# Kernel tuning notes

Hardware: AMD Instinct MI355X
Metric: run time of the kernel (lower is better)

The kernel has to match this reference:

```python
import jax, jax.numpy as jnp
import numpy as np

D_MODEL = 1024
H = 16
DK = D_MODEL // H
S = 4096


def setup_inputs() -> dict:
    key = jax.random.key(0)
    ks = jax.random.split(key, 11)
    scale = 1.0 / np.sqrt(D_MODEL)
    return {
        "Q": jax.random.normal(ks[0], (S, D_MODEL), jnp.float32),
        "K": jax.random.normal(ks[1], (S, D_MODEL), jnp.float32),
        "V": jax.random.normal(ks[2], (S, D_MODEL), jnp.float32),
        # per-head projection weights, stacked: [h, d_model, d_k]
        "Wq": jax.random.normal(ks[3], (H, D_MODEL, DK), jnp.float32) * scale,
        "bq": jax.random.normal(ks[4], (H, DK), jnp.float32) * 0.01,
        "Wk": jax.random.normal(ks[5], (H, D_MODEL, DK), jnp.float32) * scale,
        "bk": jax.random.normal(ks[6], (H, DK), jnp.float32) * 0.01,
        "Wv": jax.random.normal(ks[7], (H, D_MODEL, DK), jnp.float32) * scale,
        "bv": jax.random.normal(ks[8], (H, DK), jnp.float32) * 0.01,
        # output projection (torch Linear convention: y = x @ Wo.T + bo)
        "Wo": jax.random.normal(ks[9], (D_MODEL, D_MODEL), jnp.float32) * scale,
        "bo": jax.random.normal(ks[10], (D_MODEL,), jnp.float32) * 0.01,
    }


def reference(Q, K, V, Wq, bq, Wk, bk, Wv, bv, Wo, bo):
    # per-head projections, vectorized over heads: [h, S, d_k]
    q = jnp.einsum("sd,hdk->hsk", Q, Wq) + bq[:, None, :]
    k = jnp.einsum("sd,hdk->hsk", K, Wk) + bk[:, None, :]
    v = jnp.einsum("sd,hdk->hsk", V, Wv) + bv[:, None, :]
    # scaled dot-product attention (full [h, S, S] scores, as in the original)
    scores = jnp.einsum("hsk,htk->hst", q, k) / jnp.sqrt(jnp.float32(DK))
    attn = jax.nn.softmax(scores, axis=-1)
    o = jnp.einsum("hst,htk->hsk", attn, v)
    # concat heads along feature dim: [S, h*d_k]
    x = jnp.transpose(o, (1, 0, 2)).reshape(S, D_MODEL)
    return x @ Wo.T + bo
```

## Files before the change

### kernel.cpp

```cpp
#include <hip/hip_runtime.h>

typedef unsigned short u16;
typedef unsigned int u32;
using f32x4 = __attribute__((ext_vector_type(4))) float;
using f32x16 = __attribute__((ext_vector_type(16))) float;
using u32x4 = __attribute__((ext_vector_type(4))) u32;
using bf16x8 = __attribute__((ext_vector_type(8))) __bf16;

#define DEV __device__ __forceinline__

DEV u16 f2bf(float f) {
  u32 x = __builtin_bit_cast(u32, f);
  return (u16)((x + 0x7fffu + ((x >> 16) & 1u)) >> 16);
}

DEV f32x4 mfma16(bf16x8 a, bf16x8 b, f32x4 c) {
  return __builtin_amdgcn_mfma_f32_16x16x32_bf16(a, b, c, 0, 0, 0);
}
DEV f32x16 mfma32(bf16x8 a, bf16x8 b, f32x16 c) {
  return __builtin_amdgcn_mfma_f32_32x32x16_bf16(a, b, c, 0, 0, 0);
}

DEV float ex2(float x) {
#if __has_builtin(__builtin_amdgcn_exp2f)
  return __builtin_amdgcn_exp2f(x);
#else
  float r;
  asm("v_exp_f32 %0, %1" : "=v"(r) : "v"(x));
  return r;
#endif
}

DEV int swz(int row, int byteInRow) {
  return row * 128 + ((((byteInRow >> 4) ^ (row & 7)) << 4) | (byteInRow & 15));
}

DEV u32 pkbf(float lo, float hi) {
  union { u32 u; __bf16 h[2]; } x;
  x.h[0] = (__bf16)lo; x.h[1] = (__bf16)hi;
  return x.u;
}

DEV void gload16(const u16* g, u16* l) {
  __builtin_amdgcn_global_load_lds((const __attribute__((address_space(1))) void*)g,
                                   (__attribute__((address_space(3))) void*)l, 16, 0, 0);
}

__global__ __launch_bounds__(256) void cvt4_kernel(const float* __restrict__ a0,
                                                   const float* __restrict__ a1,
                                                   const float* __restrict__ a2,
                                                   const float* __restrict__ a3,
                                                   u16* __restrict__ o0, u16* __restrict__ o1,
                                                   u16* __restrict__ o2, u16* __restrict__ o3) {
  int y = blockIdx.y;
  if (y == 3 && blockIdx.x >= 1024) return;
  const float* in = y == 0 ? a0 : y == 1 ? a1 : y == 2 ? a2 : a3;
  u16* out = y == 0 ? o0 : y == 1 ? o1 : y == 2 ? o2 : o3;
  int i = blockIdx.x * 256 + threadIdx.x;
  float4 v = ((const float4*)in)[i];
  ushort4 w;
  w.x = f2bf(v.x); w.y = f2bf(v.y); w.z = f2bf(v.z); w.w = f2bf(v.w);
  ((ushort4*)out)[i] = w;
}

__global__ __launch_bounds__(256) void wtrans_kernel(const float* __restrict__ Wq,
                                                     const float* __restrict__ Wk,
                                                     const float* __restrict__ Wv,
                                                     u16* __restrict__ Tq,
                                                     u16* __restrict__ Tk,
                                                     u16* __restrict__ Tv) {
  __shared__ u16 t[64][68];
  const float* W = blockIdx.z == 0 ? Wq : (blockIdx.z == 1 ? Wk : Wv);
  u16* T = blockIdx.z == 0 ? Tq : (blockIdx.z == 1 ? Tk : Tv);
  int h = blockIdx.y, d0 = blockIdx.x * 64;
  int tid = threadIdx.x;
#pragma unroll
  for (int i = 0; i < 4; ++i) {
    int c = i * 256 + tid;
    int r = c >> 4, c4 = (c & 15) * 4;
    float4 v = *(const float4*)(W + h * 65536 + (d0 + r) * 64 + c4);
    t[r][c4] = f2bf(v.x); t[r][c4 + 1] = f2bf(v.y);
    t[r][c4 + 2] = f2bf(v.z); t[r][c4 + 3] = f2bf(v.w);
  }
  __syncthreads();
#pragma unroll
  for (int i = 0; i < 4; ++i) {
    int ch = i * 256 + tid;
    int cc = ch >> 4, d4 = (ch & 15) * 4;
    ushort4 w;
    w.x = t[d4][cc]; w.y = t[d4 + 1][cc]; w.z = t[d4 + 2][cc]; w.w = t[d4 + 3][cc];
    *(ushort4*)(T + (h * 64 + cc) * 1024 + d0 + d4) = w;
  }
}

__global__ __launch_bounds__(256, 3) void gemm_qkv(
    const u16* __restrict__ Qb, const u16* __restrict__ Kb, const u16* __restrict__ Vb,
    const u16* __restrict__ Tq, const u16* __restrict__ Tk, const u16* __restrict__ Tv,
    const float* __restrict__ bq, const float* __restrict__ bk, const float* __restrict__ bv,
    u16* __restrict__ qh, u16* __restrict__ kh, u16* __restrict__ vTh, float sc) {
  __shared__ alignas(16) u16 lA[128 * 64];
  __shared__ alignas(16) u16 lB[128 * 64];
  int z = blockIdx.z;
  const u16* A = z == 0 ? Qb : z == 1 ? Kb : Vb;
  const u16* B = z == 0 ? Tq : z == 1 ? Tk : Tv;
  const float* bias = z == 0 ? bq : z == 1 ? bk : bv;
  int bm = blockIdx.x, bn = blockIdx.y;
  const char* gA = (const char*)(A + bm * 131072);
  const char* gB = (const char*)(B + bn * 131072);
  int tid = threadIdx.x;
  int wid = tid >> 6, lane = tid & 63, g = lane >> 4, ln = lane & 15;
  int wr = wid >> 1, wc = wid & 1;
  const char* sA[4]; const char* sB[4];
  u16* dA[4]; u16* dB[4];
#pragma unroll
  for (int i = 0; i < 4; ++i) {
    int c = i * 256 + tid, row = c >> 3, cc = c & 7;
    int sw = (cc ^ (row & 7)) << 4;
    sA[i] = gA + row * 2048 + sw;
    sB[i] = gB + row * 2048 + sw;
    dA[i] = (u16*)((char*)lA + i * 4096 + wid * 1024);
    dB[i] = (u16*)((char*)lB + i * 4096 + wid * 1024);
  }
  f32x4 acc[4][4] = {};
  for (int k0 = 0; k0 < 1024; k0 += 64) {
#pragma unroll
    for (int i = 0; i < 4; ++i) {
      gload16((const u16*)(sA[i] + k0 * 2), dA[i]);
      gload16((const u16*)(sB[i] + k0 * 2), dB[i]);
    }
    __syncthreads();
#pragma unroll
    for (int ks = 0; ks < 2; ++ks) {
      bf16x8 af[4], bfr[4];
#pragma unroll
      for (int mt = 0; mt < 4; ++mt) {
        int row = wr * 64 + mt * 16 + ln;
        af[mt] = *(const bf16x8*)((const char*)lA + swz(row, ks * 64 + g * 16));
      }
#pragma unroll
      for (int nt = 0; nt < 4; ++nt) {
        int row = wc * 64 + nt * 16 + ln;
        bfr[nt] = *(const bf16x8*)((const char*)lB + swz(row, ks * 64 + g * 16));
      }
#pragma unroll
      for (int mt = 0; mt < 4; ++mt)
#pragma unroll
        for (int nt = 0; nt < 4; ++nt)
          acc[mt][nt] = mfma16(af[mt], bfr[nt], acc[mt][nt]);
    }
    __syncthreads();
  }
  float scale = z == 0 ? sc : 1.f;
  float bv_[4];
#pragma unroll
  for (int nt = 0; nt < 4; ++nt) bv_[nt] = bias[bn * 128 + wc * 64 + nt * 16 + ln];
  if (z < 2) {
    u16* out = z == 0 ? qh : kh;
#pragma unroll
    for (int mt = 0; mt < 4; ++mt)
      for (int nt = 0; nt < 4; ++nt)
        for (int r = 0; r < 4; ++r) {
          int s = bm * 128 + wr * 64 + mt * 16 + g * 4 + r;
          int j = bn * 128 + wc * 64 + nt * 16 + ln;
          out[(j >> 6) * 262144 + s * 64 + (j & 63)] = f2bf((acc[mt][nt][r] + bv_[nt]) * scale);
        }
  } else {
#pragma unroll
    for (int mt = 0; mt < 4; ++mt)
      for (int nt = 0; nt < 4; ++nt) {
        int sb = bm * 128 + wr * 64 + mt * 16 + g * 4;
        int j = bn * 128 + wc * 64 + nt * 16 + ln;
        ushort4 w;
        w.x = f2bf(acc[mt][nt][0] + bv_[nt]);
        w.y = f2bf(acc[mt][nt][1] + bv_[nt]);
        w.z = f2bf(acc[mt][nt][2] + bv_[nt]);
        w.w = f2bf(acc[mt][nt][3] + bv_[nt]);
        *(ushort4*)(vTh + j * 4096 + sb) = w;
      }
  }
}

__global__ __launch_bounds__(256) void gemm_out(const u16* __restrict__ A,
                                                const u16* __restrict__ B,
                                                const float* __restrict__ bias,
                                                float* __restrict__ out) {
  __shared__ alignas(16) u16 lA[64 * 64];
  __shared__ alignas(16) u16 lB[128 * 64];
  int tid = threadIdx.x;
  int wid = tid >> 6, lane = tid & 63, g = lane >> 4, ln = lane & 15;
  int wr = wid >> 1, wc = wid & 1;
  int bm = blockIdx.x, bn = blockIdx.y;
  const char* gA = (const char*)(A + bm * 65536);
  const char* gB = (const char*)(B + bn * 131072);
  const char* sA[2]; const char* sB[4];
  u16* dA[2]; u16* dB[4];
#pragma unroll
  for (int i = 0; i < 4; ++i) {
    int c = i * 256 + tid, row = c >> 3, cc = c & 7;
    int sw = (cc ^ (row & 7)) << 4;
    if (i < 2) {
      sA[i] = gA + row * 2048 + sw;
      dA[i] = (u16*)((char*)lA + i * 4096 + wid * 1024);
    }
    sB[i] = gB + row * 2048 + sw;
    dB[i] = (u16*)((char*)lB + i * 4096 + wid * 1024);
  }
  f32x4 acc[2][4] = {};
  for (int k0 = 0; k0 < 1024; k0 += 64) {
#pragma unroll
    for (int i = 0; i < 2; ++i) gload16((const u16*)(sA[i] + k0 * 2), dA[i]);
#pragma unroll
    for (int i = 0; i < 4; ++i) gload16((const u16*)(sB[i] + k0 * 2), dB[i]);
    __syncthreads();
#pragma unroll
    for (int ks = 0; ks < 2; ++ks) {
      bf16x8 af[2], bfr[4];
#pragma unroll
      for (int mt = 0; mt < 2; ++mt) {
        int row = wr * 32 + mt * 16 + ln;
        af[mt] = *(const bf16x8*)((const char*)lA + swz(row, ks * 64 + g * 16));
      }
#pragma unroll
      for (int nt = 0; nt < 4; ++nt) {
        int row = wc * 64 + nt * 16 + ln;
        bfr[nt] = *(const bf16x8*)((const char*)lB + swz(row, ks * 64 + g * 16));
      }
#pragma unroll
      for (int mt = 0; mt < 2; ++mt)
#pragma unroll
        for (int nt = 0; nt < 4; ++nt)
          acc[mt][nt] = mfma16(af[mt], bfr[nt], acc[mt][nt]);
    }
    __syncthreads();
  }
  float bv_[4];
#pragma unroll
  for (int nt = 0; nt < 4; ++nt) bv_[nt] = bias[bn * 128 + wc * 64 + nt * 16 + ln];
#pragma unroll
  for (int mt = 0; mt < 2; ++mt)
    for (int nt = 0; nt < 4; ++nt)
      for (int r = 0; r < 4; ++r) {
        int s = bm * 64 + wr * 32 + mt * 16 + g * 4 + r;
        int j = bn * 128 + wc * 64 + nt * 16 + ln;
        out[s * 1024 + j] = acc[mt][nt][r] + bv_[nt];
      }
}

__global__ __launch_bounds__(512, 4) void flash_attn2(const u16* __restrict__ qh,
                                                      const u16* __restrict__ kh,
                                                      const u16* __restrict__ vT,
                                                      u16* __restrict__ x) {
  __shared__ alignas(16) char smem[66048];
  u16* lK = (u16*)smem;
  u16* lV = (u16*)(smem + 32768);
  float* lbuf = (float*)(smem + 65536);
  float* mergeBuf = (float*)smem;

  int tid = threadIdx.x;
  int wid = tid >> 6, lane = tid & 63;
  int grp = wid >> 2, sw = wid & 3;
  int lq = lane & 31, hi = lane >> 5;
  int nb = (blockIdx.x & 7) * 64 + (blockIdx.x >> 3);
  int h = nb >> 5, qt = nb & 31;

  const u16* gK = kh + h * 262144 + grp * 131072;
  const u16* gV = vT + h * 262144 + grp * 2048;
  u16* lKg = lK + grp * 8192;
  u16* lVg = lV + grp * 8192;

  bf16x8 qf[4];
  {
    const u16* gQ = qh + h * 262144 + (qt * 128 + sw * 32 + lq) * 64 + hi * 8;
#pragma unroll
    for (int st = 0; st < 4; ++st) qf[st] = *(const bf16x8*)(gQ + st * 16);
  }
  f32x16 o0 = {}, o1 = {}, ol = {};
  u32x4 onesw;
  onesw[0] = onesw[1] = onesw[2] = onesw[3] = 0x3F803F80u;
  bf16x8 ones = __builtin_bit_cast(bf16x8, onesw);

  int r8 = lane >> 3, pc = lane & 7;
  int rowA = sw * 16 + r8, rowB = rowA + 8;
  const u16* pKA = gK + rowA * 64 + ((pc ^ (rowA & 7)) << 3);
  const u16* pKB = gK + rowB * 64 + ((pc ^ (rowB & 7)) << 3);
  const u16* pVA = gV + rowA * 4096 + ((pc ^ (rowA & 7)) << 3);
  const u16* pVB = gV + rowB * 4096 + ((pc ^ (rowB & 7)) << 3);
  u16* dKA = lKg + (sw * 16) * 64;
  u16* dKB = dKA + 512;
  u16* dVA = lVg + (sw * 16) * 64;
  u16* dVB = dVA + 512;

  gload16(pKA, dKA); gload16(pKB, dKB);
  gload16(pVA, dVA); gload16(pVB, dVB);
  pKA += 4096; pKB += 4096;
  pVA += 64; pVB += 64;

  const int NT = 32;
  for (int t = 0; t < NT; ++t) {
    asm volatile("s_waitcnt vmcnt(0)" ::: "memory");
    __builtin_amdgcn_s_barrier();
    __builtin_amdgcn_sched_barrier(0);
    int cur = t & 1;
    if (t + 1 < NT) {
      int nxt = (cur ^ 1) * 4096;
      gload16(pKA, dKA + nxt); gload16(pKB, dKB + nxt);
      gload16(pVA, dVA + nxt); gload16(pVB, dVB + nxt);
      pKA += 4096; pKB += 4096; pVA += 64; pVB += 64;
    }
    const u16* lKc = lKg + cur * 4096;
    const u16* lVc = lVg + cur * 4096;
    f32x16 s0 = {}, s1 = {};
    __builtin_amdgcn_s_setprio(1);
#pragma unroll
    for (int st = 0; st < 4; ++st) {
      bf16x8 k0 = *(const bf16x8*)((const char*)lKc + swz(lq, st * 32 + hi * 16));
      bf16x8 k1 = *(const bf16x8*)((const char*)lKc + swz(32 + lq, st * 32 + hi * 16));
      s0 = mfma32(k0, qf[st], s0);
      s1 = mfma32(k1, qf[st], s1);
    }
    __builtin_amdgcn_s_setprio(0);
#pragma unroll
    for (int r = 0; r < 16; ++r) {
      s0[r] = ex2(s0[r]);
      s1[r] = ex2(s1[r]);
    }
    bf16x8 pa[4];
#pragma unroll
    for (int n = 0; n < 2; ++n)
#pragma unroll
      for (int b2 = 0; b2 < 2; ++b2) {
        int b = b2 * 8;
        u32x4 wv;
        if (n == 0) {
          wv[0] = pkbf(s0[b + 0], s0[b + 1]); wv[1] = pkbf(s0[b + 2], s0[b + 3]);
          wv[2] = pkbf(s0[b + 4], s0[b + 5]); wv[3] = pkbf(s0[b + 6], s0[b + 7]);
        } else {
          wv[0] = pkbf(s1[b + 0], s1[b + 1]); wv[1] = pkbf(s1[b + 2], s1[b + 3]);
          wv[2] = pkbf(s1[b + 4], s1[b + 5]); wv[3] = pkbf(s1[b + 6], s1[b + 7]);
        }
        pa[n * 2 + b2] = __builtin_bit_cast(bf16x8, wv);
      }
    __builtin_amdgcn_s_setprio(1);
#pragma unroll
    for (int st = 0; st < 4; ++st) {
      uint2 a0 = *(const uint2*)((const char*)lVc + swz(lq, st * 32 + hi * 8));
      uint2 a1 = *(const uint2*)((const char*)lVc + swz(lq, st * 32 + 16 + hi * 8));
      uint2 b0 = *(const uint2*)((const char*)lVc + swz(32 + lq, st * 32 + hi * 8));
      uint2 b1 = *(const uint2*)((const char*)lVc + swz(32 + lq, st * 32 + 16 + hi * 8));
      u32x4 w0; w0[0] = a0.x; w0[1] = a0.y; w0[2] = a1.x; w0[3] = a1.y;
      u32x4 w1; w1[0] = b0.x; w1[1] = b0.y; w1[2] = b1.x; w1[3] = b1.y;
      o0 = mfma32(pa[st], __builtin_bit_cast(bf16x8, w0), o0);
      o1 = mfma32(pa[st], __builtin_bit_cast(bf16x8, w1), o1);
      ol = mfma32(pa[st], ones, ol);
    }
    __builtin_amdgcn_s_setprio(0);
  }

  __syncthreads();
  if (grp == 1) {
#pragma unroll
    for (int r = 0; r < 16; ++r) {
      int rq = (r & 3) + 8 * (r >> 2) + 4 * hi;
      float* mb = mergeBuf + (sw * 32 + rq) * 64;
      mb[lq] = o0[r];
      mb[32 + lq] = o1[r];
      if (lq == 0) lbuf[sw * 32 + rq] = ol[r];
    }
  }
  __syncthreads();
  if (grp == 0) {
#pragma unroll
    for (int r = 0; r < 16; ++r) {
      int rq = (r & 3) + 8 * (r >> 2) + 4 * hi;
      float inv = 1.f / (ol[r] + lbuf[sw * 32 + rq]);
      const float* mb = mergeBuf + (sw * 32 + rq) * 64;
      int srow = qt * 128 + sw * 32 + rq;
      u16* xr = x + srow * 1024 + h * 64;
      xr[lq] = f2bf((o0[r] + mb[lq]) * inv);
      xr[32 + lq] = f2bf((o1[r] + mb[32 + lq]) * inv);
    }
  }
}

extern "C" void kernel_launch(void* const* d_in, const int* in_sizes, int n_in,
                              void* d_out, int out_size, void* d_ws, size_t ws_size,
                              hipStream_t stream) {
  (void)in_sizes; (void)n_in; (void)out_size; (void)ws_size;
  const float* Q  = (const float*)d_in[0];
  const float* K  = (const float*)d_in[1];
  const float* V  = (const float*)d_in[2];
  const float* Wq = (const float*)d_in[3];
  const float* bq = (const float*)d_in[4];
  const float* Wk = (const float*)d_in[5];
  const float* bk = (const float*)d_in[6];
  const float* Wv = (const float*)d_in[7];
  const float* bv = (const float*)d_in[8];
  const float* Wo = (const float*)d_in[9];
  const float* bo = (const float*)d_in[10];

  char* ws = (char*)d_ws;
  u16* Qb  = (u16*)(ws + (0ull << 20));
  u16* Kb  = (u16*)(ws + (8ull << 20));
  u16* Vb  = (u16*)(ws + (16ull << 20));
  u16* Tq  = (u16*)(ws + (24ull << 20));
  u16* Tk  = (u16*)(ws + (26ull << 20));
  u16* Tv  = (u16*)(ws + (28ull << 20));
  u16* Wob = (u16*)(ws + (30ull << 20));
  u16* qh  = (u16*)(ws + (32ull << 20));
  u16* kh  = (u16*)(ws + (40ull << 20));
  u16* vTh = (u16*)(ws + (48ull << 20));
  u16* xb  = (u16*)(ws + (56ull << 20));

  const float SC = 0.125f * 1.44269504089f;

  cvt4_kernel<<<dim3(4096, 4), 256, 0, stream>>>(Q, K, V, Wo, Qb, Kb, Vb, Wob);
  wtrans_kernel<<<dim3(16, 16, 3), 256, 0, stream>>>(Wq, Wk, Wv, Tq, Tk, Tv);

  gemm_qkv<<<dim3(32, 8, 3), 256, 0, stream>>>(Qb, Kb, Vb, Tq, Tk, Tv, bq, bk, bv,
                                               qh, kh, vTh, SC);

  flash_attn2<<<512, 512, 0, stream>>>(qh, kh, vTh, xb);

  gemm_out<<<dim3(64, 8), 256, 0, stream>>>(xb, Wob, bo, (float*)d_out);
}
```

Measured before the change: 157.8 us.

## Software-pipeline flash attention so PV of previous tile overlaps QK of current

Restructures the attention inner loop so the P·V MFMAs for tile t-1 are issued right after the Q·K MFMAs for tile t, with exp2 and bf16 packing deferred until after a mid-loop barrier. K becomes single-buffered and V triple-buffered, with loads issued after the mid-loop barrier, and a tail step handles the final PV. The aim is to keep the matrix units busy while the exponentials run and to hide load latency. The cost is an extra barrier per iteration and more live registers for the carried P fragments, which may pressure occupancy at 4 waves-per-EU bounds.

Result: slower. 171.4 us (+8.6%).

```diff
diff --git a/kernel.cpp b/kernel.cpp
--- a/kernel.cpp
+++ b/kernel.cpp
@@ -246,13 +246,13 @@
       }
 }
 
-__global__ __launch_bounds__(512, 4) void flash_attn2(const u16* __restrict__ qh,
+__global__ __launch_bounds__(512, 4) void flash_attn6(const u16* __restrict__ qh,
                                                       const u16* __restrict__ kh,
                                                       const u16* __restrict__ vT,
                                                       u16* __restrict__ x) {
   __shared__ alignas(16) char smem[66048];
   u16* lK = (u16*)smem;
-  u16* lV = (u16*)(smem + 32768);
+  u16* lV = (u16*)(smem + 16384);
   float* lbuf = (float*)(smem + 65536);
   float* mergeBuf = (float*)smem;
 
@@ -265,8 +265,8 @@
 
   const u16* gK = kh + h * 262144 + grp * 131072;
   const u16* gV = vT + h * 262144 + grp * 2048;
-  u16* lKg = lK + grp * 8192;
-  u16* lVg = lV + grp * 8192;
+  u16* lKg = lK + grp * 4096;
+  u16* lVg = lV + grp * 3 * 4096;
 
   bf16x8 qf[4];
   {
@@ -291,40 +291,61 @@
   u16* dVB = dVA + 512;
 
   gload16(pKA, dKA); gload16(pKB, dKB);
+  pKA += 4096; pKB += 4096;
   gload16(pVA, dVA); gload16(pVB, dVB);
-  pKA += 4096; pKB += 4096;
   pVA += 64; pVB += 64;
+  gload16(pVA, dVA + 4096); gload16(pVB, dVB + 4096);
+  pVA += 64; pVB += 64;
+
+  bf16x8 pa[4];
 
   const int NT = 32;
   for (int t = 0; t < NT; ++t) {
     asm volatile("s_waitcnt vmcnt(0)" ::: "memory");
     __builtin_amdgcn_s_barrier();
     __builtin_amdgcn_sched_barrier(0);
-    int cur = t & 1;
-    if (t + 1 < NT) {
-      int nxt = (cur ^ 1) * 4096;
-      gload16(pKA, dKA + nxt); gload16(pKB, dKB + nxt);
-      gload16(pVA, dVA + nxt); gload16(pVB, dVB + nxt);
-      pKA += 4096; pKB += 4096; pVA += 64; pVB += 64;
-    }
-    const u16* lKc = lKg + cur * 4096;
-    const u16* lVc = lVg + cur * 4096;
     f32x16 s0 = {}, s1 = {};
     __builtin_amdgcn_s_setprio(1);
 #pragma unroll
     for (int st = 0; st < 4; ++st) {
-      bf16x8 k0 = *(const bf16x8*)((const char*)lKc + swz(lq, st * 32 + hi * 16));
-      bf16x8 k1 = *(const bf16x8*)((const char*)lKc + swz(32 + lq, st * 32 + hi * 16));
+      bf16x8 k0 = *(const bf16x8*)((const char*)lKg + swz(lq, st * 32 + hi * 16));
+      bf16x8 k1 = *(const bf16x8*)((const char*)lKg + swz(32 + lq, st * 32 + hi * 16));
       s0 = mfma32(k0, qf[st], s0);
       s1 = mfma32(k1, qf[st], s1);
     }
+    if (t) {
+      const u16* lVp = lVg + ((t - 1) % 3) * 4096;
+#pragma unroll
+      for (int st = 0; st < 4; ++st) {
+        uint2 a0 = *(const uint2*)((const char*)lVp + swz(lq, st * 32 + hi * 8));
+        uint2 a1 = *(const uint2*)((const char*)lVp + swz(lq, st * 32 + 16 + hi * 8));
+        uint2 b0 = *(const uint2*)((const char*)lVp + swz(32 + lq, st * 32 + hi * 8));
+        uint2 b1 = *(const uint2*)((const char*)lVp + swz(32 + lq, st * 32 + 16 + hi * 8));
+        u32x4 w0; w0[0] = a0.x; w0[1] = a0.y; w0[2] = a1.x; w0[3] = a1.y;
+        u32x4 w1; w1[0] = b0.x; w1[1] = b0.y; w1[2] = b1.x; w1[3] = b1.y;
+        o0 = mfma32(pa[st], __builtin_bit_cast(bf16x8, w0), o0);
+        o1 = mfma32(pa[st], __builtin_bit_cast(bf16x8, w1), o1);
+        ol = mfma32(pa[st], ones, ol);
+      }
+    }
     __builtin_amdgcn_s_setprio(0);
+    asm volatile("s_waitcnt lgkmcnt(0)" ::: "memory");
+    __builtin_amdgcn_s_barrier();
+    __builtin_amdgcn_sched_barrier(0);
+    if (t + 1 < NT) {
+      gload16(pKA, dKA); gload16(pKB, dKB);
+      pKA += 4096; pKB += 4096;
+    }
+    if (t + 2 < NT) {
+      int slot = ((t + 2) % 3) * 4096;
+      gload16(pVA, dVA + slot); gload16(pVB, dVB + slot);
+      pVA += 64; pVB += 64;
+    }
 #pragma unroll
     for (int r = 0; r < 16; ++r) {
       s0[r] = ex2(s0[r]);
       s1[r] = ex2(s1[r]);
     }
-    bf16x8 pa[4];
 #pragma unroll
     for (int n = 0; n < 2; ++n)
 #pragma unroll
@@ -340,13 +361,16 @@
         }
         pa[n * 2 + b2] = __builtin_bit_cast(bf16x8, wv);
       }
+  }
+  {
+    const u16* lVp = lVg + ((NT - 1) % 3) * 4096;
     __builtin_amdgcn_s_setprio(1);
 #pragma unroll
     for (int st = 0; st < 4; ++st) {
-      uint2 a0 = *(const uint2*)((const char*)lVc + swz(lq, st * 32 + hi * 8));
-      uint2 a1 = *(const uint2*)((const char*)lVc + swz(lq, st * 32 + 16 + hi * 8));
-      uint2 b0 = *(const uint2*)((const char*)lVc + swz(32 + lq, st * 32 + hi * 8));
-      uint2 b1 = *(const uint2*)((const char*)lVc + swz(32 + lq, st * 32 + 16 + hi * 8));
+      uint2 a0 = *(const uint2*)((const char*)lVp + swz(lq, st * 32 + hi * 8));
+      uint2 a1 = *(const uint2*)((const char*)lVp + swz(lq, st * 32 + 16 + hi * 8));
+      uint2 b0 = *(const uint2*)((const char*)lVp + swz(32 + lq, st * 32 + hi * 8));
+      uint2 b1 = *(const uint2*)((const char*)lVp + swz(32 + lq, st * 32 + 16 + hi * 8));
       u32x4 w0; w0[0] = a0.x; w0[1] = a0.y; w0[2] = a1.x; w0[3] = a1.y;
       u32x4 w1; w1[0] = b0.x; w1[1] = b0.y; w1[2] = b1.x; w1[3] = b1.y;
       o0 = mfma32(pa[st], __builtin_bit_cast(bf16x8, w0), o0);
@@ -419,7 +443,7 @@
   gemm_qkv<<<dim3(32, 8, 3), 256, 0, stream>>>(Qb, Kb, Vb, Tq, Tk, Tv, bq, bk, bv,
                                                qh, kh, vTh, SC);
 
-  flash_attn2<<<512, 512, 0, stream>>>(qh, kh, vTh, xb);
+  flash_attn6<<<512, 512, 0, stream>>>(qh, kh, vTh, xb);
 
   gemm_out<<<dim3(64, 8), 256, 0, stream>>>(xb, Wob, bo, (float*)d_out);
 }
```
